# Optimization experiments

Measured on AMD Instinct MI355X. Metric: run time of the kernel, lower is better.

## Reference

```python
import jax, jax.numpy as jnp
import numpy as np

EPS = 1.1920929e-07  # torch.finfo(float32).eps
TOP_K = 2
AUX_COEF = 0.01

def rmsnorm(x):
    return x * jax.lax.rsqrt(jnp.mean(x * x, axis=-1, keepdims=True) + EPS)

def setup_inputs() -> dict:
    key = jax.random.key(0)
    ks = jax.random.split(key, 8)
    B, T, C, H, E = 1, 2048, 1024, 2048, 8
    x = jax.random.normal(ks[0], (B, T, C), jnp.float32)
    gate_w = jax.random.normal(ks[1], (E, C), jnp.float32) * 0.02
    w1 = jax.random.normal(ks[2], (E, H, C), jnp.float32) * 0.02  # expert up-proj
    w2 = jax.random.normal(ks[3], (E, C, H), jnp.float32) * 0.02  # expert down-proj
    shared_gate_w = jax.random.normal(ks[4], (1, C), jnp.float32) * 0.02
    k_w = jax.random.normal(ks[5], (H, C), jnp.float32) * 0.02
    k_b = jax.random.normal(ks[6], (H,), jnp.float32) * 0.01
    v_w = jax.random.normal(ks[7], (C, H), jnp.float32) * 0.02
    v_b = jnp.zeros((C,), jnp.float32)
    return dict(x=x, gate_w=gate_w, w1=w1, w2=w2, shared_gate_w=shared_gate_w,
                k_w=k_w, k_b=k_b, v_w=v_w, v_b=v_b)

def reference(x, gate_w, w1, w2, shared_gate_w, k_w, k_b, v_w, v_b):
    B, T, C = x.shape
    xt = rmsnorm(x.reshape(-1, C))                     # [N,C]
    N = xt.shape[0]
    raw = xt @ gate_w.T                                # [N,E]
    scores = jax.nn.softmax(raw, axis=-1)
    topk_w, topk_idx = jax.lax.top_k(scores, TOP_K)    # [N,k]
    topk_w = topk_w / (jnp.sum(topk_w, axis=-1, keepdims=True) + 1e-6)
    E = scores.shape[-1]
    rows = jnp.arange(N)[:, None]
    onehot = jnp.zeros_like(scores).at[rows, topk_idx].set(1.0 / TOP_K)
    aux_loss = E * jnp.sum(jnp.mean(onehot, 0) * jnp.mean(scores, 0)) * AUX_COEF
    # dense gate matrix [N,E]: combine weight per (token, expert)
    g = jnp.zeros_like(scores).at[rows, topk_idx].add(topk_w)
    # grouped-GEMM expressed densely over experts (reference math identical)
    h = jnp.einsum('nc,ehc->neh', xt, w1)              # [N,E,H]
    h = jnp.square(jax.nn.relu(h)) * g[:, :, None]     # act + gate-combine weight
    out = jnp.einsum('neh,ech->nc', h, w2)             # [N,C]
    # shared expert: sigmoid gate * MLP (MLP re-norms its input)
    sg = jax.nn.sigmoid(xt @ shared_gate_w.T)          # [N,1]
    xs = rmsnorm(xt)
    kk = jnp.square(jax.nn.relu(xs @ k_w.T + k_b))     # [N,H]
    shared = kk @ v_w.T + v_b                          # [N,C]
    out = out + sg * shared
    return out.reshape(B, T, C), aux_loss
```

## Files before the change

kernel.cpp:

```cpp
#include <hip/hip_runtime.h>
#include <hip/hip_bf16.h>
#include <stdint.h>

typedef __bf16 bf16;
typedef bf16 bf16x8 __attribute__((ext_vector_type(8)));
typedef bf16 bf16x4 __attribute__((ext_vector_type(4)));
typedef float f32x4 __attribute__((ext_vector_type(4)));

constexpr int N = 2048;
constexpr int C = 1024;
constexpr int H = 2048;
constexpr int E = 8;
constexpr float EPS = 1.1920929e-07f;

constexpr int BM = 128, BN = 256;
constexpr int GT = 32;
constexpr int ASUB = 128 * 64;
constexpr int BSUB = 256 * 64;

constexpr int PREP_GATE = N / GT;
constexpr int PREP_RMS  = N;
constexpr int CVT_BLK   = ((E * H * C + H * C) / 4) / 1024;
constexpr int PREP_TOTAL = PREP_GATE + PREP_RMS + 2 * CVT_BLK;

constexpr int P1_UP    = E * (N / BM) * (H / BN);
constexpr int P1_KP    = (N / BM) * (H / BN);
constexpr int P1_TOTAL = P1_UP + P1_KP;

constexpr int P2_DOWN  = (E * 2) * (N / BM) * (C / BN);
constexpr int P2_VP    = (N / BM) * (C / BN) * 2;
constexpr int P2_TOTAL = P2_DOWN + P2_VP;

constexpr int COMBINE_BLK = (N * C / 4) / 256;

__device__ __forceinline__ void cvt_pair(const float* __restrict__ s1, bf16* __restrict__ d1,
                                         size_t n1, const float* __restrict__ s2,
                                         bf16* __restrict__ d2, int cbx) {
  size_t base = (size_t)cbx * 1024 + threadIdx.x;
  #pragma unroll
  for (int j = 0; j < 4; ++j) {
    size_t i = base + (size_t)j * 256;
    if (i < n1) {
      float4 v = ((const float4*)s1)[i];
      bf16x4 o = { (bf16)v.x, (bf16)v.y, (bf16)v.z, (bf16)v.w };
      ((bf16x4*)d1)[i] = o;
    } else {
      size_t k = i - n1;
      float4 v = ((const float4*)s2)[k];
      bf16x4 o = { (bf16)v.x, (bf16)v.y, (bf16)v.z, (bf16)v.w };
      ((bf16x4*)d2)[k] = o;
    }
  }
}

__global__ __launch_bounds__(256) void prep_kernel(
    const float* __restrict__ x, const float* __restrict__ gate_w,
    const float* __restrict__ sgw, const float* __restrict__ w1,
    const float* __restrict__ kw, const float* __restrict__ w2,
    const float* __restrict__ vw,
    bf16* __restrict__ xtb, float* __restrict__ rs2_arr,
    float* __restrict__ g, float* __restrict__ sgbuf,
    int* __restrict__ counts, int* __restrict__ lists,
    float* __restrict__ scoresums,
    bf16* __restrict__ w1b, bf16* __restrict__ kwb,
    bf16* __restrict__ w2b, bf16* __restrict__ vwb) {
  __shared__ float s_scores[8];
  __shared__ int   s_cnt[8];
  __shared__ int   s_base[8];
  __shared__ int   s_e1[GT], s_p1[GT], s_e2[GT], s_p2[GT];
  __shared__ float red[4];
  __shared__ float tot;
  const int bx = blockIdx.x;
  const int tid = threadIdx.x, lane = tid & 63, wave = tid >> 6;

  if (bx >= PREP_GATE + PREP_RMS + CVT_BLK) {
    cvt_pair(w2, w2b, (size_t)E * C * H / 4, vw, vwb,
             bx - PREP_GATE - PREP_RMS - CVT_BLK);
    return;
  }
  if (bx >= PREP_GATE + PREP_RMS) {
    cvt_pair(w1, w1b, (size_t)E * H * C / 4, kw, kwb, bx - PREP_GATE - PREP_RMS);
    return;
  }
  if (bx >= PREP_GATE) {
    int n = bx - PREP_GATE;
    float4 v = ((const float4*)(x + (size_t)n * C))[tid];
    float ss = v.x*v.x + v.y*v.y + v.z*v.z + v.w*v.w;
    #pragma unroll
    for (int off = 32; off > 0; off >>= 1) ss += __shfl_down(ss, off, 64);
    if (lane == 0) red[wave] = ss;
    __syncthreads();
    if (tid == 0) tot = red[0] + red[1] + red[2] + red[3];
    __syncthreads();
    float sumsq = tot;
    float rs1 = rsqrtf(sumsq * (1.f / C) + EPS);
    bf16x4 o = { (bf16)(v.x*rs1), (bf16)(v.y*rs1), (bf16)(v.z*rs1), (bf16)(v.w*rs1) };
    ((bf16x4*)(xtb + (size_t)n * C))[tid] = o;
    if (tid == 0) {
      float m2 = sumsq * rs1 * rs1 * (1.f / C);
      rs2_arr[n] = rsqrtf(m2 + EPS);
    }
    return;
  }
  if (tid < 8) { s_scores[tid] = 0.f; s_cnt[tid] = 0; }
  __syncthreads();

  const int tok0 = bx * GT + wave * (GT / 4);
  for (int tt = 0; tt < GT / 4; ++tt) {
    const int tok = tok0 + tt;
    const float* xr = x + (size_t)tok * C;
    float acc[10];
    #pragma unroll
    for (int e = 0; e < 10; e++) acc[e] = 0.f;
    #pragma unroll
    for (int k = 0; k < 16; ++k) {
      int c = k * 64 + lane;
      float xv = xr[c];
      #pragma unroll
      for (int e = 0; e < 8; e++) acc[e] = fmaf(xv, gate_w[e * 1024 + c], acc[e]);
      acc[8] = fmaf(xv, sgw[c], acc[8]);
      acc[9] = fmaf(xv, xv, acc[9]);
    }
    #pragma unroll
    for (int e = 0; e < 10; e++) {
      float v = acc[e];
      #pragma unroll
      for (int off = 32; off > 0; off >>= 1) v += __shfl_xor(v, off, 64);
      acc[e] = v;
    }
    if (lane == 0) {
      float rs1 = rsqrtf(acc[9] * (1.f / C) + EPS);
      float raw[9];
      #pragma unroll
      for (int e = 0; e < 9; e++) raw[e] = acc[e] * rs1;
      float m = raw[0];
      for (int e = 1; e < 8; e++) m = fmaxf(m, raw[e]);
      float sc[8], s = 0.f;
      for (int e = 0; e < 8; e++) { sc[e] = expf(raw[e] - m); s += sc[e]; }
      float inv = 1.f / s;
      for (int e = 0; e < 8; e++) sc[e] *= inv;
      int i1 = 0;
      for (int e = 1; e < 8; e++) if (sc[e] > sc[i1]) i1 = e;
      int i2 = -1;
      for (int e = 0; e < 8; e++) {
        if (e == i1) continue;
        if (i2 < 0 || sc[e] > sc[i2]) i2 = e;
      }
      float denom = sc[i1] + sc[i2] + 1e-6f;
      float* gr = g + (size_t)tok * E;
      #pragma unroll
      for (int e = 0; e < 8; e++) gr[e] = 0.f;
      gr[i1] = sc[i1] / denom;
      gr[i2] = sc[i2] / denom;
      sgbuf[tok] = 1.f / (1.f + expf(-raw[8]));
      for (int e = 0; e < 8; e++) atomicAdd(&s_scores[e], sc[e]);
      int lt = wave * (GT / 4) + tt;
      int p1 = atomicAdd(&s_cnt[i1], 1);
      int p2 = atomicAdd(&s_cnt[i2], 1);
      s_e1[lt] = i1; s_p1[lt] = p1;
      s_e2[lt] = i2; s_p2[lt] = p2;
    }
  }
  __syncthreads();
  if (tid < 8) {
    s_base[tid] = atomicAdd(&counts[tid], s_cnt[tid]);
    atomicAdd(&scoresums[tid], s_scores[tid]);
  }
  __syncthreads();
  if (tid < GT) {
    int tok = bx * GT + tid;
    int e1 = s_e1[tid], e2 = s_e2[tid];
    lists[e1 * N + s_base[e1] + s_p1[tid]] = (tok << 1);
    lists[e2 * N + s_base[e2] + s_p2[tid]] = (tok << 1) | 1;
  }
}

#define GLL(gp, lp)                                                             \
  __builtin_amdgcn_global_load_lds((__attribute__((address_space(1))) void*)(gp), \
                                   (__attribute__((address_space(3))) void*)(lp), 16, 0, 0)

__device__ __forceinline__ void mfma_loop(
    const char* pA, const char* pB0, const char* pB1,
    char* As, char* Bs, int dA, int dB0, int dB1,
    int lane, int kIters, int mb, int nb, f32x4 acc[4][4]) {
  const int arow = lane & 15;
  const int koff = (lane >> 4) * 16;
  for (int kt = 0; kt < kIters; ++kt) {
    GLL(pA,       As + dA);          GLL(pA  + 64, As + ASUB + dA);
    GLL(pB0,      Bs + dB0);         GLL(pB0 + 64, Bs + BSUB + dB0);
    GLL(pB1,      Bs + dB1);         GLL(pB1 + 64, Bs + BSUB + dB1);
    pA += 128; pB0 += 128; pB1 += 128;
    __syncthreads();
    #pragma unroll
    for (int kh = 0; kh < 2; ++kh) {
      const char* Ac = As + kh * ASUB;
      const char* Bc = Bs + kh * BSUB;
      bf16x8 a[4], b[4];
      #pragma unroll
      for (int i = 0; i < 4; ++i) {
        a[i] = *(const bf16x8*)(Ac + (mb + i * 16 + arow) * 64 + koff);
        b[i] = *(const bf16x8*)(Bc + (nb + i * 16 + arow) * 64 + koff);
      }
      #pragma unroll
      for (int i = 0; i < 4; ++i)
        #pragma unroll
        for (int j = 0; j < 4; ++j)
          acc[i][j] = __builtin_amdgcn_mfma_f32_16x16x32_bf16(a[i], b[j], acc[i][j], 0, 0, 0);
    }
    __syncthreads();
  }
}

#define GEMM_VARS                                                  \
  const int tid = threadIdx.x;                                     \
  const int lane = tid & 63, wave = tid >> 6;            \
  const int mb = (wave >> 2) * 64, nb = (wave & 3) * 64;           \
  const int srow = wave * 16 + (lane >> 2);       \
  const int scb = (lane & 3) * 16;              \
  const int dA  = wave * 1024;                      \
  const int dB0 = wave * 1024;                                     \
  const int dB1 = 8192 + wave * 1024;                              \
  const int col = lane & 15, quad = lane >> 4;                     \
  f32x4 acc[4][4] = {};

__device__ __forceinline__ void run_up(
    const bf16* __restrict__ xtb, const bf16* __restrict__ w1b,
    const float* __restrict__ g, const int* __restrict__ lists,
    const int* __restrict__ counts, bf16* __restrict__ hb,
    int e, int m0, int h0, char* As, char* Bs, int* toks) {
  const int cnt = counts[e];
  if (m0 >= cnt) return;
  GEMM_VARS
  if (tid < BM) toks[tid] = lists[e * N + min(m0 + tid, cnt - 1)];
  __syncthreads();
  const char* pA  = (const char*)xtb + ((size_t)(toks[srow] >> 1) * C) * 2 + scb;
  const char* pB0 = (const char*)w1b + ((size_t)e * H * C + (size_t)(h0 + srow) * C) * 2 + scb;
  const char* pB1 = (const char*)w1b + ((size_t)e * H * C + (size_t)(h0 + 128 + srow) * C) * 2 + scb;
  mfma_loop(pA, pB0, pB1, As, Bs, dA, dB0, dB1, lane, C / 64, mb, nb, acc);
  #pragma unroll
  for (int mi = 0; mi < 4; mi++) {
    #pragma unroll
    for (int r = 0; r < 4; r++) {
      int ml = mb + mi * 16 + quad * 4 + r;
      if (m0 + ml < cnt) {
        int packed = toks[ml];
        float gv = g[(size_t)(packed >> 1) * E + e];
        size_t base = (size_t)packed * H + h0 + nb;
        #pragma unroll
        for (int ni = 0; ni < 4; ni++) {
          float v = fmaxf(acc[mi][ni][r], 0.f);
          hb[base + ni * 16 + col] = (bf16)(v * v * gv);
        }
      }
    }
  }
}

__device__ __forceinline__ void run_kproj(
    const bf16* __restrict__ xtb, const bf16* __restrict__ kwb,
    const float* __restrict__ rs2, const float* __restrict__ k_b,
    bf16* __restrict__ kkb, int n0, int h0, char* As, char* Bs) {
  GEMM_VARS
  const char* pA  = (const char*)xtb + ((size_t)(n0 + srow) * C) * 2 + scb;
  const char* pB0 = (const char*)kwb + ((size_t)(h0 + srow) * C) * 2 + scb;
  const char* pB1 = (const char*)kwb + ((size_t)(h0 + 128 + srow) * C) * 2 + scb;
  mfma_loop(pA, pB0, pB1, As, Bs, dA, dB0, dB1, lane, C / 64, mb, nb, acc);
  #pragma unroll
  for (int mi = 0; mi < 4; mi++) {
    #pragma unroll
    for (int r = 0; r < 4; r++) {
      int n = n0 + mb + mi * 16 + quad * 4 + r;
      float rs = rs2[n];
      #pragma unroll
      for (int ni = 0; ni < 4; ni++) {
        int h = h0 + nb + ni * 16 + col;
        float v = fmaf(acc[mi][ni][r], rs, k_b[h]);
        v = fmaxf(v, 0.f);
        kkb[(size_t)n * H + h] = (bf16)(v * v);
      }
    }
  }
}

__device__ __forceinline__ void run_down(
    const bf16* __restrict__ hb, const bf16* __restrict__ w2b,
    const int* __restrict__ lists, const int* __restrict__ counts,
    float* __restrict__ dp, int e, int ks, int m0, int c0,
    char* As, char* Bs, int* toks) {
  const int cnt = counts[e];
  if (m0 >= cnt) return;
  GEMM_VARS
  if (tid < BM) toks[tid] = lists[e * N + min(m0 + tid, cnt - 1)];
  __syncthreads();
  const size_t kofs = (size_t)ks * (H / 2) * 2;
  const char* pA  = (const char*)hb + ((size_t)toks[srow] * H) * 2 + kofs + scb;
  const char* pB0 = (const char*)w2b + ((size_t)e * C * H + (size_t)(c0 + srow) * H) * 2 + kofs + scb;
  const char* pB1 = (const char*)w2b + ((size_t)e * C * H + (size_t)(c0 + 128 + srow) * H) * 2 + kofs + scb;
  mfma_loop(pA, pB0, pB1, As, Bs, dA, dB0, dB1, lane, (H / 2) / 64, mb, nb, acc);
  #pragma unroll
  for (int mi = 0; mi < 4; mi++) {
    #pragma unroll
    for (int r = 0; r < 4; r++) {
      int ml = mb + mi * 16 + quad * 4 + r;
      if (m0 + ml < cnt) {
        int packed = toks[ml];
        int tok = packed >> 1, par = packed & 1;
        float* orow = dp + (((size_t)(ks * 2 + par) * N + tok) * C) + c0 + nb;
        #pragma unroll
        for (int ni = 0; ni < 4; ni++) orow[ni * 16 + col] = acc[mi][ni][r];
      }
    }
  }
}

__device__ __forceinline__ void run_vproj(
    const bf16* __restrict__ kkb, const bf16* __restrict__ vwb,
    float* __restrict__ vp, int n0, int c0, int ks, char* As, char* Bs) {
  GEMM_VARS
  const size_t kofs = (size_t)ks * (H / 2) * 2;
  const char* pA  = (const char*)kkb + ((size_t)(n0 + srow) * H) * 2 + kofs + scb;
  const char* pB0 = (const char*)vwb + ((size_t)(c0 + srow) * H) * 2 + kofs + scb;
  const char* pB1 = (const char*)vwb + ((size_t)(c0 + 128 + srow) * H) * 2 + kofs + scb;
  mfma_loop(pA, pB0, pB1, As, Bs, dA, dB0, dB1, lane, (H / 2) / 64, mb, nb, acc);
  #pragma unroll
  for (int mi = 0; mi < 4; mi++) {
    #pragma unroll
    for (int r = 0; r < 4; r++) {
      int n = n0 + mb + mi * 16 + quad * 4 + r;
      float* orow = vp + ((size_t)ks * N + n) * C + c0 + nb;
      #pragma unroll
      for (int ni = 0; ni < 4; ni++) orow[ni * 16 + col] = acc[mi][ni][r];
    }
  }
}

__global__ __launch_bounds__(512) void phase1_kernel(
    const bf16* __restrict__ xtb, const bf16* __restrict__ w1b,
    const float* __restrict__ g, const int* __restrict__ lists,
    const int* __restrict__ counts, bf16* __restrict__ hb,
    const bf16* __restrict__ kwb, const float* __restrict__ rs2,
    const float* __restrict__ k_b, bf16* __restrict__ kkb) {
  __shared__ __align__(16) char As[2 * ASUB];
  __shared__ __align__(16) char Bs[2 * BSUB];
  __shared__ int toks[BM];
  const int bx = blockIdx.x;
  if (bx < P1_UP) {
    int e = bx >> 7, rem = bx & 127;
    int h0 = (rem & 7) * BN, m0 = (rem >> 3) * BM;
    run_up(xtb, w1b, g, lists, counts, hb, e, m0, h0, As, Bs, toks);
  } else {
    int rem = bx - P1_UP;
    int n0 = (rem & 15) * BM, h0 = (rem >> 4) * BN;
    run_kproj(xtb, kwb, rs2, k_b, kkb, n0, h0, As, Bs);
  }
}

__global__ __launch_bounds__(512) void phase2_kernel(
    const bf16* __restrict__ hb, const bf16* __restrict__ w2b,
    const int* __restrict__ lists, const int* __restrict__ counts,
    const bf16* __restrict__ kkb, const bf16* __restrict__ vwb,
    float* __restrict__ dp, float* __restrict__ vp) {
  __shared__ __align__(16) char As[2 * ASUB];
  __shared__ __align__(16) char Bs[2 * BSUB];
  __shared__ int toks[BM];
  const int bx = blockIdx.x;
  if (bx < P2_DOWN) {
    int z = bx >> 6, rem = bx & 63;
    int e = z >> 1, ks = z & 1;
    int c0 = (rem & 3) * BN, m0 = (rem >> 2) * BM;
    run_down(hb, w2b, lists, counts, dp, e, ks, m0, c0, As, Bs, toks);
  } else {
    int rem = bx - P2_DOWN;
    int ks = rem >> 6, r2 = rem & 63;
    int n0 = (r2 & 15) * BM, c0 = (r2 >> 4) * BN;
    run_vproj(kkb, vwb, vp, n0, c0, ks, As, Bs);
  }
}

__global__ __launch_bounds__(256) void combine_kernel(
    const float* __restrict__ dp, const float* __restrict__ vp,
    const float* __restrict__ v_b, const float* __restrict__ sg,
    const float* __restrict__ scoresums, const int* __restrict__ counts,
    float* __restrict__ out) {
  constexpr size_t NC = (size_t)N * C;
  if (blockIdx.x == 0 && threadIdx.x == 0) {
    float a = 0.f;
    for (int e = 0; e < 8; e++)
      a += (0.5f * (float)counts[e] * (1.f / N)) * (scoresums[e] * (1.f / N));
    out[NC] = 8.f * a * 0.01f;
  }
  size_t i = (size_t)blockIdx.x * 256 + threadIdx.x;
  size_t off = i * 4;
  int n = (int)(off >> 10);
  int c = (int)(off & 1023);
  float4 a = ((const float4*)(dp))[i];
  float4 b = ((const float4*)(dp + NC))[i];
  float4 d2 = ((const float4*)(dp + 2 * NC))[i];
  float4 d3 = ((const float4*)(dp + 3 * NC))[i];
  float4 u = ((const float4*)(vp))[i];
  float4 w = ((const float4*)(vp + NC))[i];
  float4 bias = *(const float4*)(v_b + c);
  float s = sg[n];
  float4 o;
  o.x = a.x + b.x + d2.x + d3.x + s * (u.x + w.x + bias.x);
  o.y = a.y + b.y + d2.y + d3.y + s * (u.y + w.y + bias.y);
  o.z = a.z + b.z + d2.z + d3.z + s * (u.z + w.z + bias.z);
  o.w = a.w + b.w + d2.w + d3.w + s * (u.w + w.w + bias.w);
  ((float4*)out)[i] = o;
}

extern "C" void kernel_launch(void* const* d_in, const int* in_sizes, int n_in,
                              void* d_out, int out_size, void* d_ws, size_t ws_size,
                              hipStream_t stream) {
  (void)in_sizes; (void)n_in; (void)ws_size; (void)out_size;
  const float* x   = (const float*)d_in[0];
  const float* gw  = (const float*)d_in[1];
  const float* w1  = (const float*)d_in[2];
  const float* w2  = (const float*)d_in[3];
  const float* sgw = (const float*)d_in[4];
  const float* k_w = (const float*)d_in[5];
  const float* k_b = (const float*)d_in[6];
  const float* v_w = (const float*)d_in[7];
  const float* v_b = (const float*)d_in[8];
  float* out = (float*)d_out;

  char* p = (char*)d_ws;
  auto alloc = [&](size_t bytes) { char* r = p; p += (bytes + 255) & ~255ull; return r; };
  bf16* xtb  = (bf16*)alloc((size_t)N * C * 2);
  bf16* w1b  = (bf16*)alloc((size_t)E * H * C * 2);
  bf16* w2b  = (bf16*)alloc((size_t)E * C * H * 2);
  bf16* kwb  = (bf16*)alloc((size_t)H * C * 2);
  bf16* vwb  = (bf16*)alloc((size_t)C * H * 2);
  bf16* hb   = (bf16*)alloc((size_t)2 * N * H * 2);
  bf16* kkb  = (bf16*)alloc((size_t)N * H * 2);
  float* rs2 = (float*)alloc((size_t)N * 4);
  float* g   = (float*)alloc((size_t)N * E * 4);
  float* sg  = (float*)alloc((size_t)N * 4);
  float* scoresums = (float*)alloc(256);
  int* counts = (int*)alloc(256);
  int* lists  = (int*)alloc((size_t)E * N * 4);
  float* vp   = (float*)alloc((size_t)2 * N * C * 4);
  float* dp   = (float*)w1b;

  hipMemsetAsync(scoresums, 0, 512, stream);
  prep_kernel<<<PREP_TOTAL, 256, 0, stream>>>(
      x, gw, sgw, w1, k_w, w2, v_w, xtb, rs2, g, sg, counts, lists, scoresums,
      w1b, kwb, w2b, vwb);
  phase1_kernel<<<P1_TOTAL, 512, 0, stream>>>(
      xtb, w1b, g, lists, counts, hb, kwb, rs2, k_b, kkb);
  phase2_kernel<<<P2_TOTAL, 512, 0, stream>>>(
      hb, w2b, lists, counts, kkb, vwb, dp, vp);
  combine_kernel<<<COMBINE_BLK, 256, 0, stream>>>(
      dp, vp, v_b, sg, scoresums, counts, out);
}
```

Baseline: 288.2 us.

## Overlap w2/v_w bf16 conversion with phase1 GEMMs and use wave-per-row RMSnorm

```diff
diff --git a/kernel.cpp b/kernel.cpp
--- a/kernel.cpp
+++ b/kernel.cpp
@@ -18,14 +18,15 @@
 constexpr int ASUB = 128 * 64;
 constexpr int BSUB = 256 * 64;
 
-constexpr int PREP_GATE = N / GT;
-constexpr int PREP_RMS  = N;
-constexpr int CVT_BLK   = ((E * H * C + H * C) / 4) / 1024;
-constexpr int PREP_TOTAL = PREP_GATE + PREP_RMS + 2 * CVT_BLK;
+constexpr int PREP_GATE = 64;
+constexpr int PREP_RMS  = N / 4;
+constexpr int CVT_F4    = (E * H * C + H * C) / 4;
+constexpr int CVT_BLK   = CVT_F4 / 2048;
+constexpr int PREP_TOTAL = PREP_GATE + PREP_RMS + CVT_BLK;
 
 constexpr int P1_UP    = E * (N / BM) * (H / BN);
 constexpr int P1_KP    = (N / BM) * (H / BN);
-constexpr int P1_TOTAL = P1_UP + P1_KP;
+constexpr int P1_TOTAL = P1_UP + P1_KP + CVT_BLK;
 
 constexpr int P2_DOWN  = (E * 2) * (N / BM) * (C / BN);
 constexpr int P2_VP    = (N / BM) * (C / BN) * 2;
@@ -33,13 +34,15 @@
 
 constexpr int COMBINE_BLK = (N * C / 4) / 256;
 
-__device__ __forceinline__ void cvt_pair(const float* __restrict__ s1, bf16* __restrict__ d1,
+template <int NTHR>
+__device__ __forceinline__ void cvt_item(const float* __restrict__ s1, bf16* __restrict__ d1,
                                          size_t n1, const float* __restrict__ s2,
-                                         bf16* __restrict__ d2, int cbx) {
-  size_t base = (size_t)cbx * 1024 + threadIdx.x;
+                                         bf16* __restrict__ d2, int item) {
+  constexpr int ITERS = 2048 / NTHR;
+  size_t base = (size_t)item * 2048 + threadIdx.x;
   #pragma unroll
-  for (int j = 0; j < 4; ++j) {
-    size_t i = base + (size_t)j * 256;
+  for (int j = 0; j < ITERS; ++j) {
+    size_t i = base + (size_t)j * NTHR;
     if (i < n1) {
       float4 v = ((const float4*)s1)[i];
       bf16x4 o = { (bf16)v.x, (bf16)v.y, (bf16)v.z, (bf16)v.w };
@@ -56,48 +59,45 @@
 __global__ __launch_bounds__(256) void prep_kernel(
     const float* __restrict__ x, const float* __restrict__ gate_w,
     const float* __restrict__ sgw, const float* __restrict__ w1,
-    const float* __restrict__ kw, const float* __restrict__ w2,
-    const float* __restrict__ vw,
+    const float* __restrict__ kw,
     bf16* __restrict__ xtb, float* __restrict__ rs2_arr,
     float* __restrict__ g, float* __restrict__ sgbuf,
     int* __restrict__ counts, int* __restrict__ lists,
     float* __restrict__ scoresums,
-    bf16* __restrict__ w1b, bf16* __restrict__ kwb,
-    bf16* __restrict__ w2b, bf16* __restrict__ vwb) {
+    bf16* __restrict__ w1b, bf16* __restrict__ kwb) {
   __shared__ float s_scores[8];
   __shared__ int   s_cnt[8];
   __shared__ int   s_base[8];
   __shared__ int   s_e1[GT], s_p1[GT], s_e2[GT], s_p2[GT];
-  __shared__ float red[4];
-  __shared__ float tot;
   const int bx = blockIdx.x;
   const int tid = threadIdx.x, lane = tid & 63, wave = tid >> 6;
 
-  if (bx >= PREP_GATE + PREP_RMS + CVT_BLK) {
-    cvt_pair(w2, w2b, (size_t)E * C * H / 4, vw, vwb,
-             bx - PREP_GATE - PREP_RMS - CVT_BLK);
+  if (bx >= PREP_GATE + PREP_RMS) {
+    cvt_item<256>(w1, w1b, (size_t)E * H * C / 4, kw, kwb, bx - PREP_GATE - PREP_RMS);
     return;
   }
-  if (bx >= PREP_GATE + PREP_RMS) {
-    cvt_pair(w1, w1b, (size_t)E * H * C / 4, kw, kwb, bx - PREP_GATE - PREP_RMS);
-    return;
-  }
   if (bx >= PREP_GATE) {
-    int n = bx - PREP_GATE;
-    float4 v = ((const float4*)(x + (size_t)n * C))[tid];
-    float ss = v.x*v.x + v.y*v.y + v.z*v.z + v.w*v.w;
-    #pragma unroll
-    for (int off = 32; off > 0; off >>= 1) ss += __shfl_down(ss, off, 64);
-    if (lane == 0) red[wave] = ss;
-    __syncthreads();
-    if (tid == 0) tot = red[0] + red[1] + red[2] + red[3];
-    __syncthreads();
-    float sumsq = tot;
-    float rs1 = rsqrtf(sumsq * (1.f / C) + EPS);
-    bf16x4 o = { (bf16)(v.x*rs1), (bf16)(v.y*rs1), (bf16)(v.z*rs1), (bf16)(v.w*rs1) };
-    ((bf16x4*)(xtb + (size_t)n * C))[tid] = o;
-    if (tid == 0) {
-      float m2 = sumsq * rs1 * rs1 * (1.f / C);
+    int n = (bx - PREP_GATE) * 4 + wave;
+    const float4* xr = (const float4*)(x + (size_t)n * C);
+    float4 v[4];
+    float ss = 0.f;
+    #pragma unroll
+    for (int j = 0; j < 4; ++j) {
+      v[j] = xr[j * 64 + lane];
+      ss += v[j].x * v[j].x + v[j].y * v[j].y + v[j].z * v[j].z + v[j].w * v[j].w;
+    }
+    #pragma unroll
+    for (int off = 32; off > 0; off >>= 1) ss += __shfl_xor(ss, off, 64);
+    float rs1 = rsqrtf(ss * (1.f / C) + EPS);
+    bf16x4* ot = (bf16x4*)(xtb + (size_t)n * C);
+    #pragma unroll
+    for (int j = 0; j < 4; ++j) {
+      bf16x4 o = { (bf16)(v[j].x * rs1), (bf16)(v[j].y * rs1),
+                   (bf16)(v[j].z * rs1), (bf16)(v[j].w * rs1) };
+      ot[j * 64 + lane] = o;
+    }
+    if (lane == 0) {
+      float m2 = ss * rs1 * rs1 * (1.f / C);
       rs2_arr[n] = rsqrtf(m2 + EPS);
     }
     return;
@@ -339,7 +339,9 @@
     const float* __restrict__ g, const int* __restrict__ lists,
     const int* __restrict__ counts, bf16* __restrict__ hb,
     const bf16* __restrict__ kwb, const float* __restrict__ rs2,
-    const float* __restrict__ k_b, bf16* __restrict__ kkb) {
+    const float* __restrict__ k_b, bf16* __restrict__ kkb,
+    const float* __restrict__ w2, const float* __restrict__ vw,
+    bf16* __restrict__ w2b, bf16* __restrict__ vwb) {
   __shared__ __align__(16) char As[2 * ASUB];
   __shared__ __align__(16) char Bs[2 * BSUB];
   __shared__ int toks[BM];
@@ -348,10 +350,12 @@
     int e = bx >> 7, rem = bx & 127;
     int h0 = (rem & 7) * BN, m0 = (rem >> 3) * BM;
     run_up(xtb, w1b, g, lists, counts, hb, e, m0, h0, As, Bs, toks);
-  } else {
+  } else if (bx < P1_UP + P1_KP) {
     int rem = bx - P1_UP;
     int n0 = (rem & 15) * BM, h0 = (rem >> 4) * BN;
     run_kproj(xtb, kwb, rs2, k_b, kkb, n0, h0, As, Bs);
+  } else {
+    cvt_item<512>(w2, w2b, (size_t)E * C * H / 4, vw, vwb, bx - P1_UP - P1_KP);
   }
 }
 
@@ -444,10 +448,9 @@
 
   hipMemsetAsync(scoresums, 0, 512, stream);
   prep_kernel<<<PREP_TOTAL, 256, 0, stream>>>(
-      x, gw, sgw, w1, k_w, w2, v_w, xtb, rs2, g, sg, counts, lists, scoresums,
-      w1b, kwb, w2b, vwb);
+      x, gw, sgw, w1, k_w, xtb, rs2, g, sg, counts, lists, scoresums, w1b, kwb);
   phase1_kernel<<<P1_TOTAL, 512, 0, stream>>>(
-      xtb, w1b, g, lists, counts, hb, kwb, rs2, k_b, kkb);
+      xtb, w1b, g, lists, counts, hb, kwb, rs2, k_b, kkb, w2, v_w, w2b, vwb);
   phase2_kernel<<<P2_TOTAL, 512, 0, stream>>>(
       hb, w2b, lists, counts, kkb, vwb, dp, vp);
   combine_kernel<<<COMBINE_BLK, 256, 0, stream>>>(
```

New measurement: 292.7 us. No clear change (+1.6%).
